# Optimization experiments

Measured on AMD Instinct MI355X. Metric: run time of the kernel, lower is better.

## Reference

```python
import jax, jax.numpy as jnp
import numpy as np

N_NODES = 50000
N_EDGES = 500000
NFEAT = 128
NHID = 128
NOUT = 16


def setup_inputs() -> dict:
    key = jax.random.key(0)
    ks = jax.random.split(key, 8)
    x = jax.random.normal(ks[0], (N_NODES, NFEAT), dtype=jnp.float32)
    edge_src = jax.random.randint(ks[1], (N_EDGES,), 0, N_NODES, dtype=jnp.int32)
    edge_dst = jax.random.randint(ks[2], (N_EDGES,), 0, N_NODES, dtype=jnp.int32)
    edge_weight = jax.random.uniform(ks[3], (N_EDGES,), dtype=jnp.float32)
    # Glorot-ish init for linear weights, zero bias (PyG GCNConv default bias=0)
    def glorot(k, fan_in, fan_out):
        s = jnp.sqrt(6.0 / (fan_in + fan_out))
        return jax.random.uniform(k, (fan_in, fan_out), jnp.float32, -s, s)
    W1 = glorot(ks[4], NFEAT, NHID)
    W2 = glorot(ks[5], NHID, NHID)
    W3 = glorot(ks[6], NHID, NOUT)
    b1 = jnp.zeros((NHID,), jnp.float32)
    b2 = jnp.zeros((NHID,), jnp.float32)
    b3 = jnp.zeros((NOUT,), jnp.float32)
    return {"x": x, "edge_src": edge_src, "edge_dst": edge_dst,
            "edge_weight": edge_weight, "W1": W1, "b1": b1,
            "W2": W2, "b2": b2, "W3": W3, "b3": b3}


def gcn_conv(x, src, dst, ew, W, b):
    """PyG GCNConv: symmetric-normalized aggregation with self-loops (weight 1).

    out_i = sum_{(j->i)} d_i^{-1/2} w_ji d_j^{-1/2} (x_j W) + d_i^{-1} (x_i W) + b
    where d_i = 1 + sum of incoming edge weights.
    """
    n = x.shape[0]
    xw = x @ W                                            # [N, F_out]
    deg = jax.ops.segment_sum(ew, dst, num_segments=n) + 1.0  # self-loop weight 1
    dinv = jnp.where(deg > 0, jax.lax.rsqrt(deg), 0.0)    # d^{-1/2}
    norm = dinv[src] * ew * dinv[dst]                     # [E]
    agg = jax.ops.segment_sum(xw[src] * norm[:, None], dst, num_segments=n)
    self_loop = xw * (dinv * dinv)[:, None]               # d_i^{-1} * x_i W
    return agg + self_loop + b


def reference(x, edge_src, edge_dst, edge_weight, W1, b1, W2, b2, W3, b3):
    # Dropout layers are identity in eval mode.
    h = gcn_conv(x, edge_src, edge_dst, edge_weight, W1, b1)
    h = jax.nn.relu(h)
    h = gcn_conv(h, edge_src, edge_dst, edge_weight, W2, b2)
    h = jax.nn.relu(h)
    h = gcn_conv(h, edge_src, edge_dst, edge_weight, W3, b3)
    return jax.nn.log_softmax(h, axis=1)
```

## Files before the change

### kernel.cpp

```cpp
#include <hip/hip_runtime.h>
#include <math.h>

#define NN 50000
#define NE 500000
#define NF 128
#define NO 16
#define SCAN_B 1024
#define NB_SCAN 49
#define NPART 16
#define EB4 489
#define EB2 977

static_assert(NN < 65536, "src must fit u16");

typedef _Float16 f16x8 __attribute__((ext_vector_type(8)));
typedef _Float16 f16x4 __attribute__((ext_vector_type(4)));
typedef float f32x4 __attribute__((ext_vector_type(4)));

union HU { unsigned short u; _Float16 h; };

__device__ inline float rec_w(unsigned int rec) {
    HU cu; cu.u = (unsigned short)(rec >> 16);
    return (float)cu.h;
}


__global__ __launch_bounds__(256) void k_count_rank(const int* __restrict__ dst,
                                                    int* __restrict__ pcnt,
                                                    int* __restrict__ rank, int E,
                                                    const float* __restrict__ W1,
                                                    const float* __restrict__ W2,
                                                    _Float16* __restrict__ W1T,
                                                    _Float16* __restrict__ W2T) {
    int b = blockIdx.x;
    if (b < EB4 - 1) {
        int part = b & (NPART - 1);
        int e0 = b * 1024 + threadIdx.x;
        int d0 = dst[e0], d1 = dst[e0 + 256], d2 = dst[e0 + 512], d3 = dst[e0 + 768];
        int r0 = atomicAdd(&pcnt[part * NN + d0], 1);
        int r1 = atomicAdd(&pcnt[part * NN + d1], 1);
        int r2 = atomicAdd(&pcnt[part * NN + d2], 1);
        int r3 = atomicAdd(&pcnt[part * NN + d3], 1);
        rank[e0]       = r0;
        rank[e0 + 256] = r1;
        rank[e0 + 512] = r2;
        rank[e0 + 768] = r3;
    } else if (b == EB4 - 1) {
        int part = b & (NPART - 1);
#pragma unroll
        for (int k = 0; k < 4; ++k) {
            int e = b * 1024 + k * 256 + threadIdx.x;
            if (e < E) {
                int d = dst[e];
                rank[e] = atomicAdd(&pcnt[part * NN + d], 1);
            }
        }
    } else {
        int idx = (b - EB4) * 256 + threadIdx.x;
        int r = idx >> 7, c = idx & 127;
        W1T[(size_t)c * NF + r] = (_Float16)W1[idx];
        W2T[(size_t)c * NF + r] = (_Float16)W2[idx];
    }
}

__global__ void k_scan1f(int* __restrict__ pcnt, int* __restrict__ offs_p,
                         int* __restrict__ bsums, int* __restrict__ done) {
    __shared__ int sm[SCAN_B];
    __shared__ int isLast;
    int t = threadIdx.x;
    int i = blockIdx.x * SCAN_B + t;
    int c = 0;
    if (i < NN) {
        int run = 0;
#pragma unroll
        for (int p = 0; p < NPART; ++p) {
            int v = pcnt[p * NN + i];
            pcnt[p * NN + i] = run;
            run += v;
        }
        c = run;
    }
    sm[t] = c;
    __syncthreads();
    for (int off = 1; off < SCAN_B; off <<= 1) {
        int x = (t >= off) ? sm[t - off] : 0;
        __syncthreads();
        sm[t] += x;
        __syncthreads();
    }
    if (i < NN) offs_p[i] = sm[t] - c;
    if (t == SCAN_B - 1) {
        __hip_atomic_store(&bsums[blockIdx.x], sm[t], __ATOMIC_RELEASE,
                           __HIP_MEMORY_SCOPE_AGENT);
        int old = __hip_atomic_fetch_add(done, 1, __ATOMIC_ACQ_REL,
                                         __HIP_MEMORY_SCOPE_AGENT);
        isLast = (old == (int)gridDim.x - 1) ? 1 : 0;
    }
    __syncthreads();
    if (isLast && t < 64) {
        int v = (t < NB_SCAN) ? __hip_atomic_load(&bsums[t], __ATOMIC_ACQUIRE,
                                                  __HIP_MEMORY_SCOPE_AGENT) : 0;
        int orig = v;
#pragma unroll
        for (int off = 1; off < 64; off <<= 1) {
            int u = __shfl_up(v, off, 64);
            if (t >= off) v += u;
        }
        if (t < NB_SCAN)
            __hip_atomic_store(&bsums[t], v - orig, __ATOMIC_RELEASE,
                               __HIP_MEMORY_SCOPE_AGENT);
    }
}

__global__ __launch_bounds__(256) void k_scatter(const int* __restrict__ src,
                                                 const int* __restrict__ dst,
                                                 const float* __restrict__ ew,
                                                 const int* __restrict__ pcnt,
                                                 const int* __restrict__ rank,
                                                 const int* __restrict__ offs_p,
                                                 const int* __restrict__ bsums,
                                                 unsigned int* __restrict__ erec, int E) {
    int b = blockIdx.x;
#pragma unroll
    for (int k = 0; k < 2; ++k) {
        int e = b * 512 + k * 256 + threadIdx.x;
        if (e < E) {
            int part = (e >> 10) & (NPART - 1);
            int d = dst[e];
            int pos = offs_p[d] + bsums[d >> 10] + pcnt[part * NN + d] + rank[e];
            HU cu; cu.h = (_Float16)ew[e];
            erec[pos] = (unsigned int)src[e] | ((unsigned int)cu.u << 16);
        }
    }
}

__global__ void k_dinv_csr(const unsigned int* __restrict__ erec,
                           const int* __restrict__ offs_p, const int* __restrict__ bsums,
                           float* __restrict__ dinv) {
    int n = blockIdx.x * blockDim.x + threadIdx.x;
    if (n < NN) {
        int s = offs_p[n] + bsums[n >> 10];
        int e = (n + 1 < NN) ? offs_p[n + 1] + bsums[(n + 1) >> 10] : NE;
        float deg = 1.0f;
        for (int j = s; j < e; ++j) deg += rec_w(erec[j]);
        dinv[n] = rsqrtf(deg);
    }
}


__device__ inline f16x8 afrag_load(const float* X, int row, int k0) {
    const float4* p = (const float4*)(X + (size_t)row * NF + k0);
    float4 a = p[0], b = p[1];
    f16x8 r;
    r[0] = (_Float16)a.x; r[1] = (_Float16)a.y; r[2] = (_Float16)a.z; r[3] = (_Float16)a.w;
    r[4] = (_Float16)b.x; r[5] = (_Float16)b.y; r[6] = (_Float16)b.z; r[7] = (_Float16)b.w;
    return r;
}
__device__ inline f16x8 afrag_load(const _Float16* X, int row, int k0) {
    return *(const f16x8*)(X + (size_t)row * NF + k0);
}

template <typename TA>
__global__ __launch_bounds__(256) void k_gemm_mfma(const TA* __restrict__ X,
                                                   const _Float16* __restrict__ WT,
                                                   const float* __restrict__ dinv,
                                                   _Float16* __restrict__ Z, int M) {
    __shared__ _Float16 ls[4][16 * 136];
    const int tid  = threadIdx.x;
    const int w    = tid >> 6;
    const int lane = tid & 63;
    const int n16  = lane & 15;
    const int quad = lane >> 4;
    const int r0   = blockIdx.x * 64 + w * 16;

    int arow = r0 + n16; if (arow > M - 1) arow = M - 1;

    f32x4 acc[8];
#pragma unroll
    for (int c = 0; c < 8; ++c) acc[c] = (f32x4){0.f, 0.f, 0.f, 0.f};

#pragma unroll
    for (int kk = 0; kk < 4; ++kk) {
        int k0 = kk * 32 + quad * 8;
        f16x8 a = afrag_load(X, arow, k0);
#pragma unroll
        for (int c = 0; c < 8; ++c) {
            f16x8 b = *(const f16x8*)(WT + (size_t)(c * 16 + n16) * NF + k0);
            acc[c] = __builtin_amdgcn_mfma_f32_16x16x32_f16(a, b, acc[c], 0, 0, 0);
        }
    }

#pragma unroll
    for (int reg = 0; reg < 4; ++reg) {
        int lrow = quad * 4 + reg;
        int grow = r0 + lrow; if (grow > M - 1) grow = M - 1;
        float di = dinv[grow];
#pragma unroll
        for (int c = 0; c < 8; ++c)
            ls[w][lrow * 136 + c * 16 + n16] = (_Float16)(acc[c][reg] * di);
    }
    __syncthreads();
#pragma unroll
    for (int i = 0; i < 4; ++i) {
        int off16 = i * 64 + lane;
        int row = off16 >> 4;
        int col = off16 & 15;
        int grow = r0 + row;
        if (grow < M) {
            f16x8 v = *(const f16x8*)(&ls[w][row * 136 + col * 8]);
            *(f16x8*)(Z + (size_t)grow * NF + col * 8) = v;
        }
    }
}

__global__ __launch_bounds__(256) void k_agg128h(const _Float16* __restrict__ z,
                                                 const float* __restrict__ dinv,
                                                 const int* __restrict__ offs_p,
                                                 const int* __restrict__ bsums,
                                                 const unsigned int* __restrict__ erec,
                                                 const float* __restrict__ bias,
                                                 _Float16* __restrict__ hout, int relu) {
    const int tid  = threadIdx.x;
    const int lane = tid & 63;
    const int half = lane >> 5;
    const int li   = lane & 31;
    int n = __builtin_amdgcn_readfirstlane(blockIdx.x * 4 + (tid >> 6));

    float acc0 = 0.f, acc1 = 0.f, acc2 = 0.f, acc3 = 0.f;

    int s = offs_p[n] + bsums[n >> 10];
    int e = (n + 1 < NN) ? offs_p[n + 1] + bsums[(n + 1) >> 10] : NE;
    for (int base = s; base < e; base += 64) {
        int cnt = e - base; if (cnt > 64) cnt = 64;
        unsigned int rec = 0u;
        if (lane < cnt) rec = __builtin_nontemporal_load(erec + base + lane);
        int   my_s = rec & 0xFFFF;
        float my_w = rec_w(rec);
        int cm1 = cnt - 1;
        for (int k = 0; k < cnt; k += 16) {
            int   sv[8];
            float wv[8];
            f16x4 v[8];
#pragma unroll
            for (int t = 0; t < 8; ++t) {
                int ei = k + 2 * t + half;
                int ec = ei < cm1 ? ei : cm1;
                sv[t] = __shfl(my_s, ec, 64);
                float wt = __shfl(my_w, ec, 64);
                wv[t] = (ei < cnt) ? wt : 0.0f;
            }
#pragma unroll
            for (int t = 0; t < 8; ++t)
                v[t] = *(const f16x4*)(z + ((size_t)sv[t] << 7) + li * 4);
#pragma unroll
            for (int t = 0; t < 8; ++t) {
                acc0 = fmaf((float)v[t][0], wv[t], acc0);
                acc1 = fmaf((float)v[t][1], wv[t], acc1);
                acc2 = fmaf((float)v[t][2], wv[t], acc2);
                acc3 = fmaf((float)v[t][3], wv[t], acc3);
            }
        }
    }
    acc0 += __shfl_xor(acc0, 32, 64);
    acc1 += __shfl_xor(acc1, 32, 64);
    acc2 += __shfl_xor(acc2, 32, 64);
    acc3 += __shfl_xor(acc3, 32, 64);

    f16x4 sv = *(const f16x4*)(z + ((size_t)n << 7) + li * 4);
    float di = dinv[n];
    float4 bb = *(const float4*)(bias + li * 4);
    float r0 = fmaf(di, (float)sv[0] + acc0, bb.x);
    float r1 = fmaf(di, (float)sv[1] + acc1, bb.y);
    float r2 = fmaf(di, (float)sv[2] + acc2, bb.z);
    float r3 = fmaf(di, (float)sv[3] + acc3, bb.w);
    if (relu) {
        r0 = fmaxf(r0, 0.0f); r1 = fmaxf(r1, 0.0f);
        r2 = fmaxf(r2, 0.0f); r3 = fmaxf(r3, 0.0f);
    }
    if (half == 0) {
        f16x4 o;
        o[0] = (_Float16)r0; o[1] = (_Float16)r1;
        o[2] = (_Float16)r2; o[3] = (_Float16)r3;
        __builtin_nontemporal_store(o, (f16x4*)(hout + ((size_t)n << 7) + li * 4));
    }
}

__global__ __launch_bounds__(256) void k_gemm16(const _Float16* __restrict__ H,
                                                const float* __restrict__ W3,
                                                const float* __restrict__ dinv,
                                                _Float16* __restrict__ Z3, int M) {
    __shared__ float Wl[NF * NO];
    __shared__ float Hs[16 * 132];
    int tid = threadIdx.x;
    for (int i = tid; i < NF * NO; i += 256) Wl[i] = W3[i];
    int n0 = blockIdx.x * 16;
    {
        int row = tid >> 4, h8 = tid & 15;
        int gr = n0 + row; if (gr > M - 1) gr = M - 1;
        f16x8 v = *(const f16x8*)(H + (size_t)gr * NF + h8 * 8);
        float4 f0 = {(float)v[0], (float)v[1], (float)v[2], (float)v[3]};
        float4 f1 = {(float)v[4], (float)v[5], (float)v[6], (float)v[7]};
        *(float4*)(&Hs[row * 132 + h8 * 8])     = f0;
        *(float4*)(&Hs[row * 132 + h8 * 8 + 4]) = f1;
    }
    __syncthreads();
    int ln = tid >> 4, c = tid & 15;
    float acc = 0.0f;
#pragma unroll 8
    for (int k = 0; k < NF; ++k) acc = fmaf(Hs[ln * 132 + k], Wl[k * NO + c], acc);
    int n = n0 + ln;
    if (n < M) Z3[(size_t)n * NO + c] = (_Float16)(acc * dinv[n]);
}

__global__ __launch_bounds__(256) void k_agg16_ls(const _Float16* __restrict__ z3,
                                                  const float* __restrict__ dinv,
                                                  const int* __restrict__ offs_p,
                                                  const int* __restrict__ bsums,
                                                  const unsigned int* __restrict__ erec,
                                                  const float* __restrict__ bias,
                                                  float* __restrict__ out) {
    int tid = threadIdx.x;
    int ln = tid >> 4, c = tid & 15;
    int n = blockIdx.x * 16 + ln;
    float acc = (float)z3[((size_t)n << 4) + c];
    int s = offs_p[n] + bsums[n >> 10];
    int e = (n + 1 < NN) ? offs_p[n + 1] + bsums[(n + 1) >> 10] : NE;
    int j = s;
    for (; j + 1 < e; j += 2) {
        unsigned int r0 = erec[j], r1 = erec[j + 1];
        acc = fmaf((float)z3[((size_t)(r0 & 0xFFFF) << 4) + c], rec_w(r0), acc);
        acc = fmaf((float)z3[((size_t)(r1 & 0xFFFF) << 4) + c], rec_w(r1), acc);
    }
    if (j < e) {
        unsigned int r0 = erec[j];
        acc = fmaf((float)z3[((size_t)(r0 & 0xFFFF) << 4) + c], rec_w(r0), acc);
    }
    acc = fmaf(dinv[n], acc, bias[c]);
    float m = acc;
#pragma unroll
    for (int off = 8; off > 0; off >>= 1) m = fmaxf(m, __shfl_xor(m, off, 16));
    float ex = expf(acc - m);
    float ss = ex;
#pragma unroll
    for (int off = 8; off > 0; off >>= 1) ss += __shfl_xor(ss, off, 16);
    out[(size_t)n * NO + c] = acc - m - logf(ss);
}


extern "C" void kernel_launch(void* const* d_in, const int* in_sizes, int n_in,
                              void* d_out, int out_size, void* d_ws, size_t ws_size,
                              hipStream_t stream) {
    const float* x   = (const float*)d_in[0];
    const int*   esrc= (const int*)  d_in[1];
    const int*   edst= (const int*)  d_in[2];
    const float* ew  = (const float*)d_in[3];
    const float* W1  = (const float*)d_in[4];
    const float* b1  = (const float*)d_in[5];
    const float* W2  = (const float*)d_in[6];
    const float* b2  = (const float*)d_in[7];
    const float* W3  = (const float*)d_in[8];
    const float* b3  = (const float*)d_in[9];
    float* out = (float*)d_out;

    char* p = (char*)d_ws;
    _Float16* z   = (_Float16*)p; p += (size_t)NN * NF * 2;
    _Float16* h   = (_Float16*)p; p += (size_t)NN * NF * 2;
    _Float16* z3  = (_Float16*)p; p += (size_t)NN * NO * 2;
    float* dinv   = (float*)p; p += (size_t)NN * 4;
    unsigned int* erec = (unsigned int*)p; p += (size_t)NE * 4;
    int*   rank   = (int*)p;   p += (size_t)NE * 4;
    int*   pcnt   = (int*)p;   p += (size_t)NPART * NN * 4;
    int*   done   = (int*)p;   p += 64;
    int*   offs_p = (int*)p;   p += (size_t)(NN + 1) * 4;
    int*   bsums  = (int*)p;   p += 256;
    _Float16* W1T = (_Float16*)p; p += (size_t)NF * NF * 2;
    _Float16* W2T = (_Float16*)p; p += (size_t)NF * NF * 2;

    hipMemsetAsync(pcnt, 0, (size_t)NPART * NN * 4 + 64, stream);

    k_count_rank<<<EB4 + 64, 256, 0, stream>>>(edst, pcnt, rank, NE, W1, W2, W1T, W2T);
    k_scan1f<<<NB_SCAN, SCAN_B, 0, stream>>>(pcnt, offs_p, bsums, done);
    k_scatter<<<EB2, 256, 0, stream>>>(esrc, edst, ew, pcnt, rank, offs_p, bsums, erec, NE);
    k_dinv_csr<<<(NN + 255) / 256, 256, 0, stream>>>(erec, offs_p, bsums, dinv);

    k_gemm_mfma<float><<<(NN + 63) / 64, 256, 0, stream>>>(x, W1T, dinv, z, NN);
    k_agg128h<<<NN / 4, 256, 0, stream>>>(z, dinv, offs_p, bsums, erec, b1, h, 1);
    k_gemm_mfma<_Float16><<<(NN + 63) / 64, 256, 0, stream>>>(h, W2T, dinv, z, NN);
    k_agg128h<<<NN / 4, 256, 0, stream>>>(z, dinv, offs_p, bsums, erec, b2, h, 1);
    k_gemm16<<<(NN + 15) / 16, 256, 0, stream>>>(h, W3, dinv, z3, NN);
    k_agg16_ls<<<NN / 16, 256, 0, stream>>>(z3, dinv, offs_p, bsums, erec, b3, out);
}
```

Baseline: 249.3 us.

## Process four nodes per wave in aggregation and parallelize degree computation

```diff
diff --git a/kernel.cpp b/kernel.cpp
--- a/kernel.cpp
+++ b/kernel.cpp
@@ -134,17 +134,21 @@
     }
 }
 
-__global__ void k_dinv_csr(const unsigned int* __restrict__ erec,
-                           const int* __restrict__ offs_p, const int* __restrict__ bsums,
-                           float* __restrict__ dinv) {
-    int n = blockIdx.x * blockDim.x + threadIdx.x;
-    if (n < NN) {
-        int s = offs_p[n] + bsums[n >> 10];
-        int e = (n + 1 < NN) ? offs_p[n + 1] + bsums[(n + 1) >> 10] : NE;
-        float deg = 1.0f;
-        for (int j = s; j < e; ++j) deg += rec_w(erec[j]);
-        dinv[n] = rsqrtf(deg);
-    }
+__global__ __launch_bounds__(256) void k_dinv_csr(const unsigned int* __restrict__ erec,
+                                                  const int* __restrict__ offs_p,
+                                                  const int* __restrict__ bsums,
+                                                  float* __restrict__ dinv) {
+    int tid = threadIdx.x;
+    int g = tid >> 4, li = tid & 15;
+    int n = blockIdx.x * 16 + g;
+    if (n >= NN) return;
+    int s = offs_p[n] + bsums[n >> 10];
+    int e = (n + 1 < NN) ? offs_p[n + 1] + bsums[(n + 1) >> 10] : NE;
+    float d = 0.f;
+    for (int j = s + li; j < e; j += 16) d += rec_w(erec[j]);
+#pragma unroll
+    for (int off = 8; off > 0; off >>= 1) d += __shfl_xor(d, off, 16);
+    if (li == 0) dinv[n] = rsqrtf(1.0f + d);
 }
 
 
@@ -224,64 +228,127 @@
     const int lane = tid & 63;
     const int half = lane >> 5;
     const int li   = lane & 31;
-    int n = __builtin_amdgcn_readfirstlane(blockIdx.x * 4 + (tid >> 6));
-
-    float acc0 = 0.f, acc1 = 0.f, acc2 = 0.f, acc3 = 0.f;
-
-    int s = offs_p[n] + bsums[n >> 10];
-    int e = (n + 1 < NN) ? offs_p[n + 1] + bsums[(n + 1) >> 10] : NE;
-    for (int base = s; base < e; base += 64) {
-        int cnt = e - base; if (cnt > 64) cnt = 64;
-        unsigned int rec = 0u;
-        if (lane < cnt) rec = __builtin_nontemporal_load(erec + base + lane);
-        int   my_s = rec & 0xFFFF;
-        float my_w = rec_w(rec);
-        int cm1 = cnt - 1;
-        for (int k = 0; k < cnt; k += 16) {
-            int   sv[8];
-            float wv[8];
-            f16x4 v[8];
-#pragma unroll
-            for (int t = 0; t < 8; ++t) {
-                int ei = k + 2 * t + half;
-                int ec = ei < cm1 ? ei : cm1;
-                sv[t] = __shfl(my_s, ec, 64);
-                float wt = __shfl(my_w, ec, 64);
-                wv[t] = (ei < cnt) ? wt : 0.0f;
+    const int nb = __builtin_amdgcn_readfirstlane(blockIdx.x * 16 + (tid >> 6) * 4);
+
+    int s[4], e[4], cnt[4];
+#pragma unroll
+    for (int j = 0; j < 4; ++j) {
+        int n = nb + j;
+        s[j] = offs_p[n] + bsums[n >> 10];
+        e[j] = (n + 1 < NN) ? offs_p[n + 1] + bsums[(n + 1) >> 10] : NE;
+        cnt[j] = e[j] - s[j];
+    }
+    int cmax = cnt[0] > cnt[1] ? cnt[0] : cnt[1];
+    cmax = cmax > cnt[2] ? cmax : cnt[2];
+    cmax = cmax > cnt[3] ? cmax : cnt[3];
+
+    float acc[4][4];
+#pragma unroll
+    for (int j = 0; j < 4; ++j)
+#pragma unroll
+        for (int c = 0; c < 4; ++c) acc[j][c] = 0.f;
+
+    f16x4 selfv[4];
+    float di[4];
+#pragma unroll
+    for (int j = 0; j < 4; ++j)
+        selfv[j] = *(const f16x4*)(z + ((size_t)(nb + j) << 7) + li * 4);
+#pragma unroll
+    for (int j = 0; j < 4; ++j) di[j] = dinv[nb + j];
+
+    if (cmax <= 64) {
+        unsigned int rec[4];
+#pragma unroll
+        for (int j = 0; j < 4; ++j) {
+            rec[j] = 0u;
+            if (lane < cnt[j]) rec[j] = __builtin_nontemporal_load(erec + s[j] + lane);
+        }
+        for (int k = 0; k < cmax; k += 16) {
+            f16x4 v[4][8];
+#pragma unroll
+            for (int j = 0; j < 4; ++j) {
+                int cm1 = cnt[j] - 1;
+#pragma unroll
+                for (int t = 0; t < 8; ++t) {
+                    int ei = k + 2 * t + half;
+                    int ec = ei < cm1 ? ei : cm1;
+                    ec = ec < 0 ? 0 : ec;
+                    int sv = __shfl((int)(rec[j] & 0xFFFF), ec, 64);
+                    v[j][t] = *(const f16x4*)(z + ((size_t)sv << 7) + li * 4);
+                }
             }
 #pragma unroll
-            for (int t = 0; t < 8; ++t)
-                v[t] = *(const f16x4*)(z + ((size_t)sv[t] << 7) + li * 4);
-#pragma unroll
-            for (int t = 0; t < 8; ++t) {
-                acc0 = fmaf((float)v[t][0], wv[t], acc0);
-                acc1 = fmaf((float)v[t][1], wv[t], acc1);
-                acc2 = fmaf((float)v[t][2], wv[t], acc2);
-                acc3 = fmaf((float)v[t][3], wv[t], acc3);
+            for (int j = 0; j < 4; ++j) {
+                int cm1 = cnt[j] - 1;
+                float wj = rec_w(rec[j]);
+#pragma unroll
+                for (int t = 0; t < 8; ++t) {
+                    int ei = k + 2 * t + half;
+                    int ec = ei < cm1 ? ei : cm1;
+                    ec = ec < 0 ? 0 : ec;
+                    float wt = __shfl(wj, ec, 64);
+                    float w = (ei < cnt[j]) ? wt : 0.0f;
+                    acc[j][0] = fmaf((float)v[j][t][0], w, acc[j][0]);
+                    acc[j][1] = fmaf((float)v[j][t][1], w, acc[j][1]);
+                    acc[j][2] = fmaf((float)v[j][t][2], w, acc[j][2]);
+                    acc[j][3] = fmaf((float)v[j][t][3], w, acc[j][3]);
+                }
             }
         }
-    }
-    acc0 += __shfl_xor(acc0, 32, 64);
-    acc1 += __shfl_xor(acc1, 32, 64);
-    acc2 += __shfl_xor(acc2, 32, 64);
-    acc3 += __shfl_xor(acc3, 32, 64);
-
-    f16x4 sv = *(const f16x4*)(z + ((size_t)n << 7) + li * 4);
-    float di = dinv[n];
+    } else {
+        for (int j = 0; j < 4; ++j) {
+            for (int base = s[j]; base < e[j]; base += 64) {
+                int cc = e[j] - base; if (cc > 64) cc = 64;
+                unsigned int rec = 0u;
+                if (lane < cc) rec = __builtin_nontemporal_load(erec + base + lane);
+                int cm1 = cc - 1;
+                float wj = rec_w(rec);
+                for (int k = 0; k < cc; k += 16) {
+                    f16x4 v[8];
+                    float w[8];
+#pragma unroll
+                    for (int t = 0; t < 8; ++t) {
+                        int ei = k + 2 * t + half;
+                        int ec = ei < cm1 ? ei : cm1;
+                        ec = ec < 0 ? 0 : ec;
+                        int sv = __shfl((int)(rec & 0xFFFF), ec, 64);
+                        float wt = __shfl(wj, ec, 64);
+                        w[t] = (ei < cc) ? wt : 0.0f;
+                        v[t] = *(const f16x4*)(z + ((size_t)sv << 7) + li * 4);
+                    }
+#pragma unroll
+                    for (int t = 0; t < 8; ++t) {
+                        acc[j][0] = fmaf((float)v[t][0], w[t], acc[j][0]);
+                        acc[j][1] = fmaf((float)v[t][1], w[t], acc[j][1]);
+                        acc[j][2] = fmaf((float)v[t][2], w[t], acc[j][2]);
+                        acc[j][3] = fmaf((float)v[t][3], w[t], acc[j][3]);
+                    }
+                }
+            }
+        }
+    }
+
     float4 bb = *(const float4*)(bias + li * 4);
-    float r0 = fmaf(di, (float)sv[0] + acc0, bb.x);
-    float r1 = fmaf(di, (float)sv[1] + acc1, bb.y);
-    float r2 = fmaf(di, (float)sv[2] + acc2, bb.z);
-    float r3 = fmaf(di, (float)sv[3] + acc3, bb.w);
-    if (relu) {
-        r0 = fmaxf(r0, 0.0f); r1 = fmaxf(r1, 0.0f);
-        r2 = fmaxf(r2, 0.0f); r3 = fmaxf(r3, 0.0f);
-    }
-    if (half == 0) {
-        f16x4 o;
-        o[0] = (_Float16)r0; o[1] = (_Float16)r1;
-        o[2] = (_Float16)r2; o[3] = (_Float16)r3;
-        __builtin_nontemporal_store(o, (f16x4*)(hout + ((size_t)n << 7) + li * 4));
+#pragma unroll
+    for (int j = 0; j < 4; ++j) {
+        float a0 = acc[j][0] + __shfl_xor(acc[j][0], 32, 64);
+        float a1 = acc[j][1] + __shfl_xor(acc[j][1], 32, 64);
+        float a2 = acc[j][2] + __shfl_xor(acc[j][2], 32, 64);
+        float a3 = acc[j][3] + __shfl_xor(acc[j][3], 32, 64);
+        float r0 = fmaf(di[j], (float)selfv[j][0] + a0, bb.x);
+        float r1 = fmaf(di[j], (float)selfv[j][1] + a1, bb.y);
+        float r2 = fmaf(di[j], (float)selfv[j][2] + a2, bb.z);
+        float r3 = fmaf(di[j], (float)selfv[j][3] + a3, bb.w);
+        if (relu) {
+            r0 = fmaxf(r0, 0.0f); r1 = fmaxf(r1, 0.0f);
+            r2 = fmaxf(r2, 0.0f); r3 = fmaxf(r3, 0.0f);
+        }
+        if (half == 0) {
+            f16x4 o;
+            o[0] = (_Float16)r0; o[1] = (_Float16)r1;
+            o[2] = (_Float16)r2; o[3] = (_Float16)r3;
+            __builtin_nontemporal_store(o, (f16x4*)(hout + ((size_t)(nb + j) << 7) + li * 4));
+        }
     }
 }
 
@@ -325,15 +392,18 @@
     float acc = (float)z3[((size_t)n << 4) + c];
     int s = offs_p[n] + bsums[n >> 10];
     int e = (n + 1 < NN) ? offs_p[n + 1] + bsums[(n + 1) >> 10] : NE;
-    int j = s;
-    for (; j + 1 < e; j += 2) {
-        unsigned int r0 = erec[j], r1 = erec[j + 1];
-        acc = fmaf((float)z3[((size_t)(r0 & 0xFFFF) << 4) + c], rec_w(r0), acc);
-        acc = fmaf((float)z3[((size_t)(r1 & 0xFFFF) << 4) + c], rec_w(r1), acc);
-    }
-    if (j < e) {
-        unsigned int r0 = erec[j];
-        acc = fmaf((float)z3[((size_t)(r0 & 0xFFFF) << 4) + c], rec_w(r0), acc);
+    for (int k = s; k < e; k += 16) {
+        float vv[16], ww[16];
+#pragma unroll
+        for (int t = 0; t < 16; ++t) {
+            int idx = k + t;
+            int ic = idx < e ? idx : e - 1;
+            unsigned int r = erec[ic];
+            vv[t] = (float)z3[((size_t)(r & 0xFFFF) << 4) + c];
+            ww[t] = (idx < e) ? rec_w(r) : 0.0f;
+        }
+#pragma unroll
+        for (int t = 0; t < 16; ++t) acc = fmaf(vv[t], ww[t], acc);
     }
     acc = fmaf(dinv[n], acc, bias[c]);
     float m = acc;
@@ -381,12 +451,12 @@
     k_count_rank<<<EB4 + 64, 256, 0, stream>>>(edst, pcnt, rank, NE, W1, W2, W1T, W2T);
     k_scan1f<<<NB_SCAN, SCAN_B, 0, stream>>>(pcnt, offs_p, bsums, done);
     k_scatter<<<EB2, 256, 0, stream>>>(esrc, edst, ew, pcnt, rank, offs_p, bsums, erec, NE);
-    k_dinv_csr<<<(NN + 255) / 256, 256, 0, stream>>>(erec, offs_p, bsums, dinv);
+    k_dinv_csr<<<(NN + 15) / 16, 256, 0, stream>>>(erec, offs_p, bsums, dinv);
 
     k_gemm_mfma<float><<<(NN + 63) / 64, 256, 0, stream>>>(x, W1T, dinv, z, NN);
-    k_agg128h<<<NN / 4, 256, 0, stream>>>(z, dinv, offs_p, bsums, erec, b1, h, 1);
+    k_agg128h<<<NN / 16, 256, 0, stream>>>(z, dinv, offs_p, bsums, erec, b1, h, 1);
     k_gemm_mfma<_Float16><<<(NN + 63) / 64, 256, 0, stream>>>(h, W2T, dinv, z, NN);
-    k_agg128h<<<NN / 4, 256, 0, stream>>>(z, dinv, offs_p, bsums, erec, b2, h, 1);
+    k_agg128h<<<NN / 16, 256, 0, stream>>>(z, dinv, offs_p, bsums, erec, b2, h, 1);
     k_gemm16<<<(NN + 15) / 16, 256, 0, stream>>>(h, W3, dinv, z3, NN);
     k_agg16_ls<<<NN / 16, 256, 0, stream>>>(z3, dinv, offs_p, bsums, erec, b3, out);
 }
```

New measurement: 257.9 us. 1.03x slower.

## Fuse degree into scatter, fold layer-3 GEMM into aggregation, unroll agg16

Applied to the files above, without the earlier changes.

```diff
diff --git a/kernel.cpp b/kernel.cpp
--- a/kernel.cpp
+++ b/kernel.cpp
@@ -119,7 +119,8 @@
                                                  const int* __restrict__ rank,
                                                  const int* __restrict__ offs_p,
                                                  const int* __restrict__ bsums,
-                                                 unsigned int* __restrict__ erec, int E) {
+                                                 unsigned int* __restrict__ erec,
+                                                 float* __restrict__ deg, int E) {
     int b = blockIdx.x;
 #pragma unroll
     for (int k = 0; k < 2; ++k) {
@@ -127,23 +128,12 @@
         if (e < E) {
             int part = (e >> 10) & (NPART - 1);
             int d = dst[e];
+            float w = ew[e];
             int pos = offs_p[d] + bsums[d >> 10] + pcnt[part * NN + d] + rank[e];
-            HU cu; cu.h = (_Float16)ew[e];
+            HU cu; cu.h = (_Float16)w;
             erec[pos] = (unsigned int)src[e] | ((unsigned int)cu.u << 16);
-        }
-    }
-}
-
-__global__ void k_dinv_csr(const unsigned int* __restrict__ erec,
-                           const int* __restrict__ offs_p, const int* __restrict__ bsums,
-                           float* __restrict__ dinv) {
-    int n = blockIdx.x * blockDim.x + threadIdx.x;
-    if (n < NN) {
-        int s = offs_p[n] + bsums[n >> 10];
-        int e = (n + 1 < NN) ? offs_p[n + 1] + bsums[(n + 1) >> 10] : NE;
-        float deg = 1.0f;
-        for (int j = s; j < e; ++j) deg += rec_w(erec[j]);
-        dinv[n] = rsqrtf(deg);
+            atomicAdd(&deg[d], w);
+        }
     }
 }
 
@@ -163,7 +153,7 @@
 template <typename TA>
 __global__ __launch_bounds__(256) void k_gemm_mfma(const TA* __restrict__ X,
                                                    const _Float16* __restrict__ WT,
-                                                   const float* __restrict__ dinv,
+                                                   const float* __restrict__ deg,
                                                    _Float16* __restrict__ Z, int M) {
     __shared__ _Float16 ls[4][16 * 136];
     const int tid  = threadIdx.x;
@@ -194,7 +184,7 @@
     for (int reg = 0; reg < 4; ++reg) {
         int lrow = quad * 4 + reg;
         int grow = r0 + lrow; if (grow > M - 1) grow = M - 1;
-        float di = dinv[grow];
+        float di = rsqrtf(1.0f + deg[grow]);
 #pragma unroll
         for (int c = 0; c < 8; ++c)
             ls[w][lrow * 136 + c * 16 + n16] = (_Float16)(acc[c][reg] * di);
@@ -213,21 +203,13 @@
     }
 }
 
-__global__ __launch_bounds__(256) void k_agg128h(const _Float16* __restrict__ z,
-                                                 const float* __restrict__ dinv,
-                                                 const int* __restrict__ offs_p,
-                                                 const int* __restrict__ bsums,
-                                                 const unsigned int* __restrict__ erec,
-                                                 const float* __restrict__ bias,
-                                                 _Float16* __restrict__ hout, int relu) {
-    const int tid  = threadIdx.x;
-    const int lane = tid & 63;
-    const int half = lane >> 5;
-    const int li   = lane & 31;
-    int n = __builtin_amdgcn_readfirstlane(blockIdx.x * 4 + (tid >> 6));
-
-    float acc0 = 0.f, acc1 = 0.f, acc2 = 0.f, acc3 = 0.f;
-
+__device__ __forceinline__ void agg_gather(const _Float16* __restrict__ z,
+                                           const int* __restrict__ offs_p,
+                                           const int* __restrict__ bsums,
+                                           const unsigned int* __restrict__ erec,
+                                           int n, int lane, int half, int li,
+                                           float& acc0, float& acc1,
+                                           float& acc2, float& acc3) {
     int s = offs_p[n] + bsums[n >> 10];
     int e = (n + 1 < NN) ? offs_p[n + 1] + bsums[(n + 1) >> 10] : NE;
     for (int base = s; base < e; base += 64) {
@@ -265,18 +247,31 @@
     acc1 += __shfl_xor(acc1, 32, 64);
     acc2 += __shfl_xor(acc2, 32, 64);
     acc3 += __shfl_xor(acc3, 32, 64);
+}
+
+__global__ __launch_bounds__(256) void k_agg128h(const _Float16* __restrict__ z,
+                                                 const float* __restrict__ deg,
+                                                 const int* __restrict__ offs_p,
+                                                 const int* __restrict__ bsums,
+                                                 const unsigned int* __restrict__ erec,
+                                                 const float* __restrict__ bias,
+                                                 _Float16* __restrict__ hout) {
+    const int tid  = threadIdx.x;
+    const int lane = tid & 63;
+    const int half = lane >> 5;
+    const int li   = lane & 31;
+    int n = __builtin_amdgcn_readfirstlane(blockIdx.x * 4 + (tid >> 6));
+
+    float acc0 = 0.f, acc1 = 0.f, acc2 = 0.f, acc3 = 0.f;
+    agg_gather(z, offs_p, bsums, erec, n, lane, half, li, acc0, acc1, acc2, acc3);
 
     f16x4 sv = *(const f16x4*)(z + ((size_t)n << 7) + li * 4);
-    float di = dinv[n];
+    float di = rsqrtf(1.0f + deg[n]);
     float4 bb = *(const float4*)(bias + li * 4);
-    float r0 = fmaf(di, (float)sv[0] + acc0, bb.x);
-    float r1 = fmaf(di, (float)sv[1] + acc1, bb.y);
-    float r2 = fmaf(di, (float)sv[2] + acc2, bb.z);
-    float r3 = fmaf(di, (float)sv[3] + acc3, bb.w);
-    if (relu) {
-        r0 = fmaxf(r0, 0.0f); r1 = fmaxf(r1, 0.0f);
-        r2 = fmaxf(r2, 0.0f); r3 = fmaxf(r3, 0.0f);
-    }
+    float r0 = fmaxf(fmaf(di, (float)sv[0] + acc0, bb.x), 0.0f);
+    float r1 = fmaxf(fmaf(di, (float)sv[1] + acc1, bb.y), 0.0f);
+    float r2 = fmaxf(fmaf(di, (float)sv[2] + acc2, bb.z), 0.0f);
+    float r3 = fmaxf(fmaf(di, (float)sv[3] + acc3, bb.w), 0.0f);
     if (half == 0) {
         f16x4 o;
         o[0] = (_Float16)r0; o[1] = (_Float16)r1;
@@ -285,35 +280,57 @@
     }
 }
 
-__global__ __launch_bounds__(256) void k_gemm16(const _Float16* __restrict__ H,
-                                                const float* __restrict__ W3,
-                                                const float* __restrict__ dinv,
-                                                _Float16* __restrict__ Z3, int M) {
-    __shared__ float Wl[NF * NO];
-    __shared__ float Hs[16 * 132];
-    int tid = threadIdx.x;
-    for (int i = tid; i < NF * NO; i += 256) Wl[i] = W3[i];
-    int n0 = blockIdx.x * 16;
-    {
-        int row = tid >> 4, h8 = tid & 15;
-        int gr = n0 + row; if (gr > M - 1) gr = M - 1;
-        f16x8 v = *(const f16x8*)(H + (size_t)gr * NF + h8 * 8);
-        float4 f0 = {(float)v[0], (float)v[1], (float)v[2], (float)v[3]};
-        float4 f1 = {(float)v[4], (float)v[5], (float)v[6], (float)v[7]};
-        *(float4*)(&Hs[row * 132 + h8 * 8])     = f0;
-        *(float4*)(&Hs[row * 132 + h8 * 8 + 4]) = f1;
-    }
+__global__ __launch_bounds__(256) void k_agg128f(const _Float16* __restrict__ z,
+                                                 const float* __restrict__ deg,
+                                                 const int* __restrict__ offs_p,
+                                                 const int* __restrict__ bsums,
+                                                 const unsigned int* __restrict__ erec,
+                                                 const float* __restrict__ bias,
+                                                 const float* __restrict__ W3,
+                                                 _Float16* __restrict__ z3) {
+    __shared__ float w3t[NO * 132];
+    const int tid  = threadIdx.x;
+    for (int i = tid; i < NF * NO; i += 256) {
+        int k = i >> 4, c = i & 15;
+        w3t[c * 132 + k + (k >> 5)] = W3[i];
+    }
+    const int lane = tid & 63;
+    const int half = lane >> 5;
+    const int li   = lane & 31;
+    int n = __builtin_amdgcn_readfirstlane(blockIdx.x * 4 + (tid >> 6));
     __syncthreads();
-    int ln = tid >> 4, c = tid & 15;
-    float acc = 0.0f;
-#pragma unroll 8
-    for (int k = 0; k < NF; ++k) acc = fmaf(Hs[ln * 132 + k], Wl[k * NO + c], acc);
-    int n = n0 + ln;
-    if (n < M) Z3[(size_t)n * NO + c] = (_Float16)(acc * dinv[n]);
+
+    float acc0 = 0.f, acc1 = 0.f, acc2 = 0.f, acc3 = 0.f;
+    agg_gather(z, offs_p, bsums, erec, n, lane, half, li, acc0, acc1, acc2, acc3);
+
+    f16x4 sv = *(const f16x4*)(z + ((size_t)n << 7) + li * 4);
+    float di = rsqrtf(1.0f + deg[n]);
+    float4 bb = *(const float4*)(bias + li * 4);
+    float r0 = fmaxf(fmaf(di, (float)sv[0] + acc0, bb.x), 0.0f);
+    float r1 = fmaxf(fmaf(di, (float)sv[1] + acc1, bb.y), 0.0f);
+    float r2 = fmaxf(fmaf(di, (float)sv[2] + acc2, bb.z), 0.0f);
+    float r3 = fmaxf(fmaf(di, (float)sv[3] + acc3, bb.w), 0.0f);
+
+    const int c = lane & 15, q = lane >> 4;
+    float p = 0.f;
+#pragma unroll
+    for (int m = 0; m < 8; ++m) {
+        int sl = q * 8 + m;
+        float h0 = __shfl(r0, sl, 64), h1 = __shfl(r1, sl, 64);
+        float h2 = __shfl(r2, sl, 64), h3 = __shfl(r3, sl, 64);
+        int kb = c * 132 + q * 33 + m * 4;
+        p = fmaf(h0, w3t[kb],     p);
+        p = fmaf(h1, w3t[kb + 1], p);
+        p = fmaf(h2, w3t[kb + 2], p);
+        p = fmaf(h3, w3t[kb + 3], p);
+    }
+    p += __shfl_xor(p, 16, 64);
+    p += __shfl_xor(p, 32, 64);
+    if (lane < 16) z3[((size_t)n << 4) + lane] = (_Float16)(p * di);
 }
 
 __global__ __launch_bounds__(256) void k_agg16_ls(const _Float16* __restrict__ z3,
-                                                  const float* __restrict__ dinv,
+                                                  const float* __restrict__ deg,
                                                   const int* __restrict__ offs_p,
                                                   const int* __restrict__ bsums,
                                                   const unsigned int* __restrict__ erec,
@@ -325,17 +342,21 @@
     float acc = (float)z3[((size_t)n << 4) + c];
     int s = offs_p[n] + bsums[n >> 10];
     int e = (n + 1 < NN) ? offs_p[n + 1] + bsums[(n + 1) >> 10] : NE;
-    int j = s;
-    for (; j + 1 < e; j += 2) {
-        unsigned int r0 = erec[j], r1 = erec[j + 1];
-        acc = fmaf((float)z3[((size_t)(r0 & 0xFFFF) << 4) + c], rec_w(r0), acc);
-        acc = fmaf((float)z3[((size_t)(r1 & 0xFFFF) << 4) + c], rec_w(r1), acc);
-    }
-    if (j < e) {
-        unsigned int r0 = erec[j];
-        acc = fmaf((float)z3[((size_t)(r0 & 0xFFFF) << 4) + c], rec_w(r0), acc);
-    }
-    acc = fmaf(dinv[n], acc, bias[c]);
+    for (int k = s; k < e; k += 16) {
+        float vv[16], ww[16];
+#pragma unroll
+        for (int t = 0; t < 16; ++t) {
+            int idx = k + t;
+            int ic = idx < e ? idx : e - 1;
+            unsigned int r = erec[ic];
+            vv[t] = (float)z3[((size_t)(r & 0xFFFF) << 4) + c];
+            ww[t] = (idx < e) ? rec_w(r) : 0.0f;
+        }
+#pragma unroll
+        for (int t = 0; t < 16; ++t) acc = fmaf(vv[t], ww[t], acc);
+    }
+    float di = rsqrtf(1.0f + deg[n]);
+    acc = fmaf(di, acc, bias[c]);
     float m = acc;
 #pragma unroll
     for (int off = 8; off > 0; off >>= 1) m = fmaxf(m, __shfl_xor(m, off, 16));
@@ -366,27 +387,25 @@
     _Float16* z   = (_Float16*)p; p += (size_t)NN * NF * 2;
     _Float16* h   = (_Float16*)p; p += (size_t)NN * NF * 2;
     _Float16* z3  = (_Float16*)p; p += (size_t)NN * NO * 2;
-    float* dinv   = (float*)p; p += (size_t)NN * 4;
     unsigned int* erec = (unsigned int*)p; p += (size_t)NE * 4;
     int*   rank   = (int*)p;   p += (size_t)NE * 4;
     int*   pcnt   = (int*)p;   p += (size_t)NPART * NN * 4;
+    float* deg    = (float*)p; p += (size_t)NN * 4;
     int*   done   = (int*)p;   p += 64;
     int*   offs_p = (int*)p;   p += (size_t)(NN + 1) * 4;
     int*   bsums  = (int*)p;   p += 256;
     _Float16* W1T = (_Float16*)p; p += (size_t)NF * NF * 2;
     _Float16* W2T = (_Float16*)p; p += (size_t)NF * NF * 2;
 
-    hipMemsetAsync(pcnt, 0, (size_t)NPART * NN * 4 + 64, stream);
+    hipMemsetAsync(pcnt, 0, (size_t)NPART * NN * 4 + (size_t)NN * 4 + 64, stream);
 
     k_count_rank<<<EB4 + 64, 256, 0, stream>>>(edst, pcnt, rank, NE, W1, W2, W1T, W2T);
     k_scan1f<<<NB_SCAN, SCAN_B, 0, stream>>>(pcnt, offs_p, bsums, done);
-    k_scatter<<<EB2, 256, 0, stream>>>(esrc, edst, ew, pcnt, rank, offs_p, bsums, erec, NE);
-    k_dinv_csr<<<(NN + 255) / 256, 256, 0, stream>>>(erec, offs_p, bsums, dinv);
-
-    k_gemm_mfma<float><<<(NN + 63) / 64, 256, 0, stream>>>(x, W1T, dinv, z, NN);
-    k_agg128h<<<NN / 4, 256, 0, stream>>>(z, dinv, offs_p, bsums, erec, b1, h, 1);
-    k_gemm_mfma<_Float16><<<(NN + 63) / 64, 256, 0, stream>>>(h, W2T, dinv, z, NN);
-    k_agg128h<<<NN / 4, 256, 0, stream>>>(z, dinv, offs_p, bsums, erec, b2, h, 1);
-    k_gemm16<<<(NN + 15) / 16, 256, 0, stream>>>(h, W3, dinv, z3, NN);
-    k_agg16_ls<<<NN / 16, 256, 0, stream>>>(z3, dinv, offs_p, bsums, erec, b3, out);
-}
+    k_scatter<<<EB2, 256, 0, stream>>>(esrc, edst, ew, pcnt, rank, offs_p, bsums, erec, deg, NE);
+
+    k_gemm_mfma<float><<<(NN + 63) / 64, 256, 0, stream>>>(x, W1T, deg, z, NN);
+    k_agg128h<<<NN / 4, 256, 0, stream>>>(z, deg, offs_p, bsums, erec, b1, h);
+    k_gemm_mfma<_Float16><<<(NN + 63) / 64, 256, 0, stream>>>(h, W2T, deg, z, NN);
+    k_agg128f<<<NN / 4, 256, 0, stream>>>(z, deg, offs_p, bsums, erec, b2, W3, z3);
+    k_agg16_ls<<<NN / 16, 256, 0, stream>>>(z3, deg, offs_p, bsums, erec, b3, out);
+}
```

After: 273.4 us. 9.6% more time.

## Widen aggregation loads, parallelize degree sum, and unroll 16-wide gather

Applied to the files above, without the earlier changes.

```diff
diff --git a/kernel.cpp b/kernel.cpp
--- a/kernel.cpp
+++ b/kernel.cpp
@@ -134,17 +134,21 @@
     }
 }
 
-__global__ void k_dinv_csr(const unsigned int* __restrict__ erec,
-                           const int* __restrict__ offs_p, const int* __restrict__ bsums,
-                           float* __restrict__ dinv) {
-    int n = blockIdx.x * blockDim.x + threadIdx.x;
-    if (n < NN) {
-        int s = offs_p[n] + bsums[n >> 10];
-        int e = (n + 1 < NN) ? offs_p[n + 1] + bsums[(n + 1) >> 10] : NE;
-        float deg = 1.0f;
-        for (int j = s; j < e; ++j) deg += rec_w(erec[j]);
-        dinv[n] = rsqrtf(deg);
-    }
+__global__ __launch_bounds__(256) void k_dinv_csr(const unsigned int* __restrict__ erec,
+                                                  const int* __restrict__ offs_p,
+                                                  const int* __restrict__ bsums,
+                                                  float* __restrict__ dinv) {
+    int tid = threadIdx.x;
+    int g = tid >> 4, li = tid & 15;
+    int n = blockIdx.x * 16 + g;
+    if (n >= NN) return;
+    int s = offs_p[n] + bsums[n >> 10];
+    int e = (n + 1 < NN) ? offs_p[n + 1] + bsums[(n + 1) >> 10] : NE;
+    float d = 0.f;
+    for (int j = s + li; j < e; j += 16) d += rec_w(erec[j]);
+#pragma unroll
+    for (int off = 8; off > 0; off >>= 1) d += __shfl_xor(d, off, 16);
+    if (li == 0) dinv[n] = rsqrtf(1.0f + d);
 }
 
 
@@ -222,66 +226,74 @@
                                                  _Float16* __restrict__ hout, int relu) {
     const int tid  = threadIdx.x;
     const int lane = tid & 63;
-    const int half = lane >> 5;
-    const int li   = lane & 31;
+    const int q    = lane >> 4;
+    const int li   = lane & 15;
     int n = __builtin_amdgcn_readfirstlane(blockIdx.x * 4 + (tid >> 6));
 
-    float acc0 = 0.f, acc1 = 0.f, acc2 = 0.f, acc3 = 0.f;
+    float acc[8];
+#pragma unroll
+    for (int j = 0; j < 8; ++j) acc[j] = 0.f;
 
     int s = offs_p[n] + bsums[n >> 10];
     int e = (n + 1 < NN) ? offs_p[n + 1] + bsums[(n + 1) >> 10] : NE;
     for (int base = s; base < e; base += 64) {
         int cnt = e - base; if (cnt > 64) cnt = 64;
         unsigned int rec = 0u;
-        if (lane < cnt) rec = __builtin_nontemporal_load(erec + base + lane);
+        if (lane < cnt) rec = erec[base + lane];
         int   my_s = rec & 0xFFFF;
         float my_w = rec_w(rec);
         int cm1 = cnt - 1;
         for (int k = 0; k < cnt; k += 16) {
-            int   sv[8];
-            float wv[8];
-            f16x4 v[8];
-#pragma unroll
-            for (int t = 0; t < 8; ++t) {
-                int ei = k + 2 * t + half;
+            int   sv[4];
+            float wv[4];
+            f16x8 v[4];
+#pragma unroll
+            for (int t = 0; t < 4; ++t) {
+                int ei = k + 4 * t + q;
                 int ec = ei < cm1 ? ei : cm1;
                 sv[t] = __shfl(my_s, ec, 64);
                 float wt = __shfl(my_w, ec, 64);
                 wv[t] = (ei < cnt) ? wt : 0.0f;
             }
 #pragma unroll
-            for (int t = 0; t < 8; ++t)
-                v[t] = *(const f16x4*)(z + ((size_t)sv[t] << 7) + li * 4);
-#pragma unroll
-            for (int t = 0; t < 8; ++t) {
-                acc0 = fmaf((float)v[t][0], wv[t], acc0);
-                acc1 = fmaf((float)v[t][1], wv[t], acc1);
-                acc2 = fmaf((float)v[t][2], wv[t], acc2);
-                acc3 = fmaf((float)v[t][3], wv[t], acc3);
+            for (int t = 0; t < 4; ++t)
+                v[t] = *(const f16x8*)(z + ((size_t)sv[t] << 7) + li * 8);
+#pragma unroll
+            for (int t = 0; t < 4; ++t) {
+#pragma unroll
+                for (int j = 0; j < 8; ++j)
+                    acc[j] = fmaf((float)v[t][j], wv[t], acc[j]);
             }
         }
     }
-    acc0 += __shfl_xor(acc0, 32, 64);
-    acc1 += __shfl_xor(acc1, 32, 64);
-    acc2 += __shfl_xor(acc2, 32, 64);
-    acc3 += __shfl_xor(acc3, 32, 64);
-
-    f16x4 sv = *(const f16x4*)(z + ((size_t)n << 7) + li * 4);
+#pragma unroll
+    for (int j = 0; j < 8; ++j) {
+        acc[j] += __shfl_xor(acc[j], 32, 64);
+        acc[j] += __shfl_xor(acc[j], 16, 64);
+    }
+
+    f16x8 sv8 = *(const f16x8*)(z + ((size_t)n << 7) + li * 8);
     float di = dinv[n];
-    float4 bb = *(const float4*)(bias + li * 4);
-    float r0 = fmaf(di, (float)sv[0] + acc0, bb.x);
-    float r1 = fmaf(di, (float)sv[1] + acc1, bb.y);
-    float r2 = fmaf(di, (float)sv[2] + acc2, bb.z);
-    float r3 = fmaf(di, (float)sv[3] + acc3, bb.w);
+    float4 bb0 = *(const float4*)(bias + li * 8);
+    float4 bb1 = *(const float4*)(bias + li * 8 + 4);
+    float r[8];
+    r[0] = fmaf(di, (float)sv8[0] + acc[0], bb0.x);
+    r[1] = fmaf(di, (float)sv8[1] + acc[1], bb0.y);
+    r[2] = fmaf(di, (float)sv8[2] + acc[2], bb0.z);
+    r[3] = fmaf(di, (float)sv8[3] + acc[3], bb0.w);
+    r[4] = fmaf(di, (float)sv8[4] + acc[4], bb1.x);
+    r[5] = fmaf(di, (float)sv8[5] + acc[5], bb1.y);
+    r[6] = fmaf(di, (float)sv8[6] + acc[6], bb1.z);
+    r[7] = fmaf(di, (float)sv8[7] + acc[7], bb1.w);
     if (relu) {
-        r0 = fmaxf(r0, 0.0f); r1 = fmaxf(r1, 0.0f);
-        r2 = fmaxf(r2, 0.0f); r3 = fmaxf(r3, 0.0f);
-    }
-    if (half == 0) {
-        f16x4 o;
-        o[0] = (_Float16)r0; o[1] = (_Float16)r1;
-        o[2] = (_Float16)r2; o[3] = (_Float16)r3;
-        __builtin_nontemporal_store(o, (f16x4*)(hout + ((size_t)n << 7) + li * 4));
+#pragma unroll
+        for (int j = 0; j < 8; ++j) r[j] = fmaxf(r[j], 0.0f);
+    }
+    if (q == 0) {
+        f16x8 o;
+#pragma unroll
+        for (int j = 0; j < 8; ++j) o[j] = (_Float16)r[j];
+        __builtin_nontemporal_store(o, (f16x8*)(hout + ((size_t)n << 7) + li * 8));
     }
 }
 
@@ -325,15 +337,18 @@
     float acc = (float)z3[((size_t)n << 4) + c];
     int s = offs_p[n] + bsums[n >> 10];
     int e = (n + 1 < NN) ? offs_p[n + 1] + bsums[(n + 1) >> 10] : NE;
-    int j = s;
-    for (; j + 1 < e; j += 2) {
-        unsigned int r0 = erec[j], r1 = erec[j + 1];
-        acc = fmaf((float)z3[((size_t)(r0 & 0xFFFF) << 4) + c], rec_w(r0), acc);
-        acc = fmaf((float)z3[((size_t)(r1 & 0xFFFF) << 4) + c], rec_w(r1), acc);
-    }
-    if (j < e) {
-        unsigned int r0 = erec[j];
-        acc = fmaf((float)z3[((size_t)(r0 & 0xFFFF) << 4) + c], rec_w(r0), acc);
+    for (int k = s; k < e; k += 16) {
+        float vv[16], ww[16];
+#pragma unroll
+        for (int t = 0; t < 16; ++t) {
+            int idx = k + t;
+            int ic = idx < e ? idx : e - 1;
+            unsigned int r = erec[ic];
+            vv[t] = (float)z3[((size_t)(r & 0xFFFF) << 4) + c];
+            ww[t] = (idx < e) ? rec_w(r) : 0.0f;
+        }
+#pragma unroll
+        for (int t = 0; t < 16; ++t) acc = fmaf(vv[t], ww[t], acc);
     }
     acc = fmaf(dinv[n], acc, bias[c]);
     float m = acc;
@@ -381,7 +396,7 @@
     k_count_rank<<<EB4 + 64, 256, 0, stream>>>(edst, pcnt, rank, NE, W1, W2, W1T, W2T);
     k_scan1f<<<NB_SCAN, SCAN_B, 0, stream>>>(pcnt, offs_p, bsums, done);
     k_scatter<<<EB2, 256, 0, stream>>>(esrc, edst, ew, pcnt, rank, offs_p, bsums, erec, NE);
-    k_dinv_csr<<<(NN + 255) / 256, 256, 0, stream>>>(erec, offs_p, bsums, dinv);
+    k_dinv_csr<<<(NN + 15) / 16, 256, 0, stream>>>(erec, offs_p, bsums, dinv);
 
     k_gemm_mfma<float><<<(NN + 63) / 64, 256, 0, stream>>>(x, W1T, dinv, z, NN);
     k_agg128h<<<NN / 4, 256, 0, stream>>>(z, dinv, offs_p, bsums, erec, b1, h, 1);
```

Result: faster. 240.1 us (-3.7%).
